# Kernel optimization log

Measured on AMD Instinct MI355X. Metric: run time of the kernel, lower is better.

The kernel has to match this reference:

```python
import jax, jax.numpy as jnp
import numpy as np

BN_EPS = 1e-5


def _weight_mlp(off, Wh, bh, Wo, bo):
    # off: [Nout, k, 2] relative neighbor offsets -> [Nout, k, 9] interp coeffs
    h = jax.nn.relu(off @ Wh + bh)
    return h @ Wo + bo


def _interp_conv(x, idx, off, Wk, bk, Wh, bh, Wo, bo):
    # x: [B, Cin, Nin]; idx: [Nout, k] neighbor indices into Nin; Wk: [Cout, Cin, 9]
    a = _weight_mlp(off, Wh, bh, Wo, bo)        # [Nout, k, 9]
    feats = x[:, :, idx]                         # gather -> [B, Cin, Nout, k]
    # dynamic filter: per-neighbor kernel = a @ Wk taps, contracted with features
    y = jnp.einsum('nkt,bcnk,oct->bon', a, feats, Wk)  # [B, Cout, Nout]
    return y + bk[None, :, None]


def _bn_relu(x, g, b):
    # BatchNorm1d over [B, C, N] using batch statistics (training-mode forward)
    mean = x.mean(axis=(0, 2), keepdims=True)
    var = x.var(axis=(0, 2), keepdims=True)
    xn = (x - mean) * jax.lax.rsqrt(var + BN_EPS)
    return jax.nn.relu(xn * g[None, :, None] + b[None, :, None])


def setup_inputs() -> dict:
    key = jax.random.key(0)
    ks = jax.random.split(key, 12)
    B, N1, N2, N3, K = 8, 50176, 12544, 3136, 9
    inp = {
        'x': jax.random.normal(ks[0], (B, 3, N1), jnp.float32),
        'nbr1': jax.random.randint(ks[1], (N2, K), 0, N1, jnp.int32),
        'off1': jax.random.normal(ks[2], (N2, K, 2), jnp.float32),
        'nbr2': jax.random.randint(ks[3], (N2, K), 0, N2, jnp.int32),
        'off2': jax.random.normal(ks[4], (N2, K, 2), jnp.float32),
        'pool_idx': jax.random.randint(ks[5], (N3, K), 0, N2, jnp.int32),
        'Wh': jax.random.normal(ks[6], (2, 32), jnp.float32) * 0.5,
        'bh': jnp.zeros((32,), jnp.float32),
        'Wo': jax.random.normal(ks[7], (32, 9), jnp.float32) * 0.2,
        'bo': jnp.zeros((9,), jnp.float32),
        'W1': jax.random.normal(ks[8], (32, 3, 9), jnp.float32) * 0.2,
        'b1': jnp.zeros((32,), jnp.float32),
        'W2': jax.random.normal(ks[9], (32, 32, 9), jnp.float32) * 0.06,
        'b2': jnp.zeros((32,), jnp.float32),
        'W3': jax.random.normal(ks[10], (64, 32, 9), jnp.float32) * 0.06,
        'b3': jnp.zeros((64,), jnp.float32),
        'g1': jnp.ones((32,), jnp.float32), 'be1': jnp.zeros((32,), jnp.float32),
        'g2': jnp.ones((32,), jnp.float32), 'be2': jnp.zeros((32,), jnp.float32),
        'g3': jnp.ones((64,), jnp.float32), 'be3': jnp.zeros((64,), jnp.float32),
    }
    return inp


def reference(x, nbr1, off1, nbr2, off2, pool_idx, Wh, bh, Wo, bo,
              W1, b1, W2, b2, W3, b3, g1, be1, g2, be2, g3, be3):
    x = _bn_relu(_interp_conv(x, nbr1, off1, W1, b1, Wh, bh, Wo, bo), g1, be1)
    x = _bn_relu(_interp_conv(x, nbr2, off2, W2, b2, Wh, bh, Wo, bo), g2, be2)
    x = _bn_relu(_interp_conv(x, nbr2, off2, W3, b3, Wh, bh, Wo, bo), g3, be3)
    # MaxPoolNG: max over irregular neighbor sets from level l2 -> l3
    x = x[:, :, pool_idx].max(axis=-1)           # [B, 64, N3]
    return x
```

## Files before the change

kernel.cpp:

```cpp
#include <hip/hip_runtime.h>
#include <math.h>

#define N1C 50176
#define N2C 12544
#define N3C 3136
#define NT_TILES (N2C * 8 / 64)

typedef __attribute__((ext_vector_type(8))) short bf16x8;
typedef __attribute__((ext_vector_type(4))) float f32x4;

__device__ __forceinline__ unsigned short f2bf(float f) {
    unsigned u = __builtin_bit_cast(unsigned, f);
    u += 0x7fffu + ((u >> 16) & 1u);
    return (unsigned short)(u >> 16);
}
__device__ __forceinline__ unsigned cvtpk(float lo, float hi) {
    unsigned r;
    asm("v_cvt_pk_bf16_f32 %0, %1, %2" : "=v"(r) : "v"(lo), "v"(hi));
    return r;
}
__device__ __forceinline__ float bf2f(unsigned short u) {
    return __builtin_bit_cast(float, (unsigned)u << 16);
}
__device__ __forceinline__ float bflo(unsigned u) {
    return __builtin_bit_cast(float, u << 16);
}
__device__ __forceinline__ float bfhi(unsigned u) {
    return __builtin_bit_cast(float, u & 0xffff0000u);
}

#define TRB (N1C / 64)
#define MLB (2 * N2C * 9 / 256)
#define PWB 112

__device__ __forceinline__ void pad_one(int i, const float* __restrict__ W,
                                        unsigned short* __restrict__ Wp,
                                        int OC, int CIN, int KT) {
    int j = i & 7;
    int op = (i >> 3) & 31;
    int q = (i >> 8) & 3;
    int kt = (i >> 10) % KT;
    int g = i / (KT * 1024);
    int kp = kt * 32 + q * 8 + j;
    int t = kp / CIN, c = kp - t * CIN;
    int o = g * 32 + op;
    float v = (t < 9 && o < OC) ? W[(o * CIN + c) * 9 + t] : 0.f;
    Wp[i] = f2bf(v);
}

__global__ void prologue_kernel(const float* __restrict__ x, unsigned short* __restrict__ X0,
                                const float* __restrict__ off1, const float* __restrict__ off2,
                                const float* __restrict__ Wh, const float* __restrict__ bh,
                                const float* __restrict__ Wo, const float* __restrict__ bo,
                                float* __restrict__ A1, float* __restrict__ A2,
                                const float* __restrict__ W1, const float* __restrict__ W2,
                                const float* __restrict__ W3,
                                unsigned short* __restrict__ W1p, unsigned short* __restrict__ W2p,
                                unsigned short* __restrict__ W3p) {
    __shared__ float U[2304];
    int blk = blockIdx.x;
    int tid = threadIdx.x;
    if (blk < TRB) {
        int n0 = blk * 64;
        for (int r = tid; r < 24 * 64; r += 256) {
            int cb = r >> 6;
            int nn = r & 63;
            U[nn * 25 + cb] = x[cb * N1C + n0 + nn];
        }
        __syncthreads();
        for (int w = tid; w < 64 * 24; w += 256) {
            int nn = w / 24;
            int u = w - nn * 24;
            X0[(n0 + nn) * 24 + u] = f2bf(U[nn * 25 + u]);
        }
    } else if (blk < TRB + MLB) {
        int bi = blk - TRB;
        int idx = bi * 256 + tid;
        const float* offp;
        if (idx < N2C * 9) offp = off1 + idx * 2;
        else offp = off2 + (idx - N2C * 9) * 2;
        float o0 = offp[0], o1 = offp[1];
        float out[9];
#pragma unroll
        for (int t = 0; t < 9; t++) out[t] = bo[t];
#pragma unroll
        for (int h = 0; h < 32; h++) {
            float hv = fmaxf(o0 * Wh[h] + o1 * Wh[32 + h] + bh[h], 0.f);
#pragma unroll
            for (int t = 0; t < 9; t++) out[t] += hv * Wo[h * 9 + t];
        }
#pragma unroll
        for (int t = 0; t < 9; t++) U[tid * 9 + t] = out[t];
        __syncthreads();
        float* dst = (bi < 441) ? (A1 + (size_t)bi * 2304)
                                : (A2 + (size_t)(bi - 441) * 2304);
        for (int i = tid; i < 2304; i += 256) dst[i] = U[i];
    } else {
        int i = (blk - TRB - MLB) * 256 + tid;
        if (i < 1024) pad_one(i, W1, W1p, 32, 3, 1);
        else if (i < 10240) pad_one(i - 1024, W2, W2p, 32, 32, 9);
        else pad_one(i - 10240, W3, W3p, 64, 32, 9);
    }
}

template <int CIN, int MW, bool HAS_BN>
__global__ __launch_bounds__(256, 4)
void conv_kernel(const unsigned short* __restrict__ Xin,
                 const int* __restrict__ nbr,
                 const float* __restrict__ A,
                 const unsigned short* __restrict__ Wp,
                 const float* __restrict__ bias,
                 const float* __restrict__ bnsc,
                 const float* __restrict__ bnsh,
                 unsigned short* __restrict__ Yb,
                 double* __restrict__ Part) {
    constexpr int OC = MW * 16;
    constexpr int KREAL = 9 * CIN;
    constexpr int KROW = (KREAL + 31) & ~31;
    constexpr int KT = KROW / 32;
    constexpr int KSTR = KROW + 8;
    constexpr int PARTS = 256 / OC;
    constexpr int PCOLS = 64 / PARTS;
    constexpr int OSH = (OC == 32) ? 5 : 6;
    constexpr int YSTR = OC + 4;
    constexpr int SB1 = 64 * KSTR * 2;
    constexpr int SB2 = 64 * YSTR * 4 + PARTS * 2 * OC * 4;
    constexpr int SBYTES = SB1 > SB2 ? SB1 : SB2;
    __shared__ alignas(16) char Sraw[SBYTES];
    __shared__ float a_lds[8 * 81];
    short* S = (short*)Sraw;

    int tid = threadIdx.x;
    int tile = blockIdx.x;
    int n0 = tile * 8;

    for (int i = tid; i < 64 * KSTR; i += 256) S[i] = 0;
    for (int i = tid; i < 648; i += 256) a_lds[i] = A[(size_t)n0 * 81 + i];
    __syncthreads();
    if (tid < 192) {
        int nsub = tid / 24;
        int u = tid - nsub * 24;
        int b = u / 3, c = u - b * 3;
        int n = n0 + nsub;
        const int* nb = nbr + n * 9;
        const float* Ar = a_lds + nsub * 81;
        float s[9];
#pragma unroll
        for (int t = 0; t < 9; t++) s[t] = 0.f;
#pragma unroll
        for (int k = 0; k < 9; k++) {
            float f = bf2f(Xin[nb[k] * 24 + u]);
#pragma unroll
            for (int t = 0; t < 9; t++) s[t] = fmaf(Ar[k * 9 + t], f, s[t]);
        }
        int col = nsub * 8 + b;
#pragma unroll
        for (int t = 0; t < 9; t++) S[col * KSTR + t * 3 + c] = (short)f2bf(s[t]);
    }
    __syncthreads();

    int lane = tid & 63, wv = tid >> 6, q = lane >> 4, cl = lane & 15;
    int colg = wv * 16 + cl;

    const bf16x8* wf = (const bf16x8*)Wp;
    f32x4 acc[MW];
#pragma unroll
    for (int m = 0; m < MW; m++) acc[m] = (f32x4){0.f, 0.f, 0.f, 0.f};
#pragma unroll
    for (int kt = 0; kt < KT; kt++) {
        bf16x8 bfr = *(const bf16x8*)&S[colg * KSTR + kt * 32 + q * 8];
#pragma unroll
        for (int m = 0; m < MW; m++) {
            const bf16x8* wg = wf + (m >> 1) * (KT * 128);
            bf16x8 am = wg[(kt * 4 + q) * 32 + cl + (m & 1) * 16];
            acc[m] = __builtin_amdgcn_mfma_f32_16x16x32_bf16(am, bfr, acc[m], 0, 0, 0);
        }
    }
    __syncthreads();

    float* Yf = (float*)Sraw;
    float* P2f = Yf + 64 * YSTR;
    int C = tile * 64 + colg;
#pragma unroll
    for (int m = 0; m < MW; m++) {
        f32x4 v;
#pragma unroll
        for (int i = 0; i < 4; i++) v[i] = acc[m][i] + bias[m * 16 + q * 4 + i];
        *(f32x4*)&Yf[colg * YSTR + m * 16 + q * 4] = v;
        uint2 pk;
        pk.x = cvtpk(v[0], v[1]);
        pk.y = cvtpk(v[2], v[3]);
        *(uint2*)&Yb[(size_t)C * OC + m * 16 + q * 4] = pk;
    }
    __syncthreads();
    {
        int o = tid & (OC - 1);
        int part = tid >> OSH;
        float s = 0.f, qq = 0.f;
#pragma unroll
        for (int i = 0; i < PCOLS; i++) {
            float y = Yf[(part * PCOLS + i) * YSTR + o];
            s += y;
            qq += y * y;
        }
        P2f[part * 2 * OC + o] = s;
        P2f[part * 2 * OC + OC + o] = qq;
    }
    __syncthreads();
    if (tid < 2 * OC) {
        double v = 0.0;
#pragma unroll
        for (int p = 0; p < PARTS; p++) v += (double)P2f[p * 2 * OC + tid];
        Part[(size_t)tid * NT_TILES + tile] = v;
    }
}

template <int MW>
__global__ __launch_bounds__(256, 4)
void conv32_kernel(const unsigned short* __restrict__ Xin,
                   const int* __restrict__ nbr,
                   const float* __restrict__ A,
                   const unsigned short* __restrict__ Wp,
                   const float* __restrict__ bias,
                   const float* __restrict__ bnsc,
                   const float* __restrict__ bnsh,
                   unsigned short* __restrict__ Yb,
                   double* __restrict__ Part) {
    constexpr int OC = MW * 16;
    constexpr int KT = 9;
    constexpr int KSTR = 296;
    constexpr int PARTS = 256 / OC;
    constexpr int PCOLS = 64 / PARTS;
    constexpr int OSH = (OC == 32) ? 5 : 6;
    constexpr int YSTR = OC + 4;
    constexpr int SB1 = 64 * KSTR * 2;
    constexpr int SB2 = 64 * YSTR * 4 + PARTS * 2 * OC * 4;
    constexpr int SBYTES = SB1 > SB2 ? SB1 : SB2;
    __shared__ alignas(16) char Sraw[SBYTES];
    __shared__ float a_lds[8 * 81];
    short* S = (short*)Sraw;

    int tid = threadIdx.x;
    int wv4 = __builtin_amdgcn_readfirstlane(tid >> 6);
    int lane = tid & 63;
    int b = lane >> 3, c4 = lane & 7;
    int wv = tid >> 6, q = lane >> 4, cl = lane & 15;
    int colg = wv * 16 + cl;
    float4 scv = *(const float4*)&bnsc[4 * c4];
    float4 shv = *(const float4*)&bnsh[4 * c4];
    const uint2* Xd = (const uint2*)Xin;
    const bf16x8* wf = (const bf16x8*)Wp;
    float* Yf = (float*)Sraw;
    float* P2f = Yf + 64 * YSTR;

#pragma unroll 1
    for (int it = 0; it < 2; ++it) {
        int tile = blockIdx.x * 2 + it;
        int n0 = tile * 8;
        if (it) __syncthreads();

        uint2 fu[18];
#pragma unroll
        for (int gg = 0; gg < 2; gg++)
#pragma unroll
            for (int k = 0; k < 9; k++) {
                int j = nbr[(n0 + wv4 * 2 + gg) * 9 + k];
                fu[gg * 9 + k] = Xd[(size_t)j * 64 + lane];
            }
        for (int i = tid; i < 648; i += 256) a_lds[i] = A[(size_t)n0 * 81 + i];
        __syncthreads();
#pragma unroll
        for (int gg = 0; gg < 2; gg++) {
            const float* Ar = a_lds + (wv4 * 2 + gg) * 81;
            float s0[9], s1[9], s2[9], s3[9];
#pragma unroll
            for (int t = 0; t < 9; t++) { s0[t] = 0.f; s1[t] = 0.f; s2[t] = 0.f; s3[t] = 0.f; }
#pragma unroll
            for (int k = 0; k < 9; k++) {
                uint2 u = fu[gg * 9 + k];
                float f0 = fmaxf(fmaf(bflo(u.x), scv.x, shv.x), 0.f);
                float f1 = fmaxf(fmaf(bfhi(u.x), scv.y, shv.y), 0.f);
                float f2 = fmaxf(fmaf(bflo(u.y), scv.z, shv.z), 0.f);
                float f3 = fmaxf(fmaf(bfhi(u.y), scv.w, shv.w), 0.f);
#pragma unroll
                for (int t = 0; t < 9; t++) {
                    float a = Ar[k * 9 + t];
                    s0[t] = fmaf(a, f0, s0[t]);
                    s1[t] = fmaf(a, f1, s1[t]);
                    s2[t] = fmaf(a, f2, s2[t]);
                    s3[t] = fmaf(a, f3, s3[t]);
                }
            }
            int col = (wv4 * 2 + gg) * 8 + b;
            uint2* Srow = (uint2*)&S[col * KSTR];
#pragma unroll
            for (int t = 0; t < 9; t++) {
                uint2 pk;
                pk.x = cvtpk(s0[t], s1[t]);
                pk.y = cvtpk(s2[t], s3[t]);
                Srow[t * 8 + c4] = pk;
            }
        }
        __syncthreads();

        f32x4 acc[MW];
#pragma unroll
        for (int m = 0; m < MW; m++) acc[m] = (f32x4){0.f, 0.f, 0.f, 0.f};
#pragma unroll
        for (int kt = 0; kt < KT; kt++) {
            bf16x8 bfr = *(const bf16x8*)&S[colg * KSTR + kt * 32 + q * 8];
#pragma unroll
            for (int m = 0; m < MW; m++) {
                const bf16x8* wg = wf + (m >> 1) * (KT * 128);
                bf16x8 am = wg[(kt * 4 + q) * 32 + cl + (m & 1) * 16];
                acc[m] = __builtin_amdgcn_mfma_f32_16x16x32_bf16(am, bfr, acc[m], 0, 0, 0);
            }
        }
        __syncthreads();

        int C = tile * 64 + colg;
#pragma unroll
        for (int m = 0; m < MW; m++) {
            f32x4 v;
#pragma unroll
            for (int i = 0; i < 4; i++) v[i] = acc[m][i] + bias[m * 16 + q * 4 + i];
            *(f32x4*)&Yf[colg * YSTR + m * 16 + q * 4] = v;
            uint2 pk;
            pk.x = cvtpk(v[0], v[1]);
            pk.y = cvtpk(v[2], v[3]);
            *(uint2*)&Yb[(size_t)C * OC + m * 16 + q * 4] = pk;
        }
        __syncthreads();
        {
            int o = tid & (OC - 1);
            int part = tid >> OSH;
            float s = 0.f, qq = 0.f;
#pragma unroll
            for (int i = 0; i < PCOLS; i++) {
                float y = Yf[(part * PCOLS + i) * YSTR + o];
                s += y;
                qq += y * y;
            }
            P2f[part * 2 * OC + o] = s;
            P2f[part * 2 * OC + OC + o] = qq;
        }
        __syncthreads();
        if (tid < 2 * OC) {
            double v = 0.0;
#pragma unroll
            for (int p = 0; p < PARTS; p++) v += (double)P2f[p * 2 * OC + tid];
            Part[(size_t)tid * NT_TILES + tile] = v;
        }
    }
}

__global__ __launch_bounds__(256, 8)
void bn_reduce(const double* __restrict__ Part,
               const float* __restrict__ g, const float* __restrict__ be,
               float* __restrict__ sc, float* __restrict__ sh, int OC) {
    int o = blockIdx.x;
    int tid = threadIdx.x;
    const double* ps = Part + (size_t)o * NT_TILES;
    const double* pq = Part + (size_t)(OC + o) * NT_TILES;
    double s = 0.0, q = 0.0;
    for (int t = tid; t < NT_TILES; t += 256) {
        s += ps[t];
        q += pq[t];
    }
#pragma unroll
    for (int d = 1; d < 64; d <<= 1) {
        s += __shfl_xor(s, d);
        q += __shfl_xor(q, d);
    }
    __shared__ double red[8];
    int wv = tid >> 6;
    if ((tid & 63) == 0) { red[wv] = s; red[4 + wv] = q; }
    __syncthreads();
    if (tid == 0) {
        double S = red[0] + red[1] + red[2] + red[3];
        double Q = red[4] + red[5] + red[6] + red[7];
        double cnt = (double)N2C * 8.0;
        double mean = S / cnt;
        double var = Q / cnt - mean * mean;
        double rs = 1.0 / sqrt(var + 1e-5);
        double scale = (double)g[o] * rs;
        sc[o] = (float)scale;
        sh[o] = (float)((double)be[o] - mean * scale);
    }
}

__global__ __launch_bounds__(256, 8)
void pool_kernel(const unsigned short* __restrict__ Y3, const int* __restrict__ pidx,
                 const float* __restrict__ sc, const float* __restrict__ sh,
                 float* __restrict__ out) {
    int m0 = blockIdx.x * 2;
    int tid = threadIdx.x;
    int o2 = tid & 31;
    int b = tid >> 5;
    float s0 = sc[2 * o2], h0 = sh[2 * o2];
    float s1 = sc[2 * o2 + 1], h1 = sh[2 * o2 + 1];
    const unsigned* Y3u = (const unsigned*)Y3;
    int j0[9], j1[9];
#pragma unroll
    for (int k = 0; k < 9; k++) {
        j0[k] = pidx[m0 * 9 + k];
        j1[k] = pidx[m0 * 9 + 9 + k];
    }
    unsigned u0[9], u1[9];
#pragma unroll
    for (int k = 0; k < 9; k++) u0[k] = Y3u[(size_t)j0[k] * 256 + tid];
#pragma unroll
    for (int k = 0; k < 9; k++) u1[k] = Y3u[(size_t)j1[k] * 256 + tid];
    float a0 = 0.f, a1 = 0.f, c0 = 0.f, c1 = 0.f;
#pragma unroll
    for (int k = 0; k < 9; k++) {
        a0 = fmaxf(a0, fmaf(bflo(u0[k]), s0, h0));
        a1 = fmaxf(a1, fmaf(bfhi(u0[k]), s1, h1));
        c0 = fmaxf(c0, fmaf(bflo(u1[k]), s0, h0));
        c1 = fmaxf(c1, fmaf(bfhi(u1[k]), s1, h1));
    }
    float2 r0 = {a0, c0};
    float2 r1 = {a1, c1};
    *(float2*)(out + (size_t)(b * 64 + 2 * o2) * 3136 + m0) = r0;
    *(float2*)(out + (size_t)(b * 64 + 2 * o2 + 1) * 3136 + m0) = r1;
}

extern "C" void kernel_launch(void* const* d_in, const int* in_sizes, int n_in,
                              void* d_out, int out_size, void* d_ws, size_t ws_size,
                              hipStream_t stream) {
    const float* x    = (const float*)d_in[0];
    const int*   nbr1 = (const int*)d_in[1];
    const float* off1 = (const float*)d_in[2];
    const int*   nbr2 = (const int*)d_in[3];
    const float* off2 = (const float*)d_in[4];
    const int*   pidx = (const int*)d_in[5];
    const float* Wh   = (const float*)d_in[6];
    const float* bh   = (const float*)d_in[7];
    const float* Wo   = (const float*)d_in[8];
    const float* bo   = (const float*)d_in[9];
    const float* W1   = (const float*)d_in[10];
    const float* b1   = (const float*)d_in[11];
    const float* W2   = (const float*)d_in[12];
    const float* b2   = (const float*)d_in[13];
    const float* W3   = (const float*)d_in[14];
    const float* b3   = (const float*)d_in[15];
    const float* g1   = (const float*)d_in[16];
    const float* be1  = (const float*)d_in[17];
    const float* g2   = (const float*)d_in[18];
    const float* be2  = (const float*)d_in[19];
    const float* g3   = (const float*)d_in[20];
    const float* be3  = (const float*)d_in[21];

    char* ws = (char*)d_ws;
    size_t off = 0;
    auto alloc = [&](size_t bytes) -> void* {
        void* p = ws + off;
        off += (bytes + 255) & ~(size_t)255;
        return p;
    };
    unsigned short* X0b = (unsigned short*)alloc((size_t)N1C * 24 * 2);
    float* A1 = (float*)alloc((size_t)N2C * 81 * 4);
    float* A2 = (float*)alloc((size_t)N2C * 81 * 4);
    unsigned short* Y1b = (unsigned short*)alloc((size_t)N2C * 8 * 32 * 2);
    unsigned short* Y2b = (unsigned short*)alloc((size_t)N2C * 8 * 32 * 2);
    unsigned short* Y3b = (unsigned short*)alloc((size_t)N2C * 8 * 64 * 2);
    unsigned short* W1p = (unsigned short*)alloc(32 * 32 * 2);
    unsigned short* W2p = (unsigned short*)alloc(32 * 288 * 2);
    unsigned short* W3p = (unsigned short*)alloc(64 * 288 * 2);
    double* Part  = (double*)alloc((size_t)NT_TILES * 128 * 8);
    float*  scbuf = (float*)alloc(256 * 4);

    float* sc1 = scbuf;       float* sh1 = scbuf + 32;
    float* sc2 = scbuf + 64;  float* sh2 = scbuf + 96;
    float* sc3 = scbuf + 128; float* sh3 = scbuf + 192;

    prologue_kernel<<<TRB + MLB + PWB, 256, 0, stream>>>(
        x, X0b, off1, off2, Wh, bh, Wo, bo, A1, A2, W1, W2, W3, W1p, W2p, W3p);

    conv_kernel<3, 2, false><<<NT_TILES, 256, 0, stream>>>(
        X0b, nbr1, A1, W1p, b1, nullptr, nullptr, Y1b, Part);
    bn_reduce<<<32, 256, 0, stream>>>(Part, g1, be1, sc1, sh1, 32);

    conv32_kernel<2><<<NT_TILES / 2, 256, 0, stream>>>(
        Y1b, nbr2, A2, W2p, b2, sc1, sh1, Y2b, Part);
    bn_reduce<<<32, 256, 0, stream>>>(Part, g2, be2, sc2, sh2, 32);

    conv32_kernel<4><<<NT_TILES / 2, 256, 0, stream>>>(
        Y2b, nbr2, A2, W3p, b3, sc2, sh2, Y3b, Part);
    bn_reduce<<<64, 256, 0, stream>>>(Part, g3, be3, sc3, sh3, 64);

    pool_kernel<<<N3C / 2, 256, 0, stream>>>(Y3b, pidx, sc3, sh3, (float*)d_out);
}
```

Before: 222.9 us.

## Split conv32 into two batch-half launches with 16-point tiles

The 32-channel dynamic-filter convolutions now run as two launches, each handling four of the eight batch images over 16-point tiles, instead of one kernel covering all eight batches over 8-point tiles in a two-iteration loop. Each thread gathers 2 channels for 4 points rather than 4 channels for 2 points. Interpolation coefficients are read straight from global memory instead of being staged in LDS. The aim is a smaller per-launch working set for the gathered features so they stay in cache, plus more reuse of the coefficient matrix per point. In exchange there is an extra launch per layer, narrower 4-byte gather loads, and the coefficient matrix is read twice.

New measurement: 204.3 us. 1.09x faster.

```diff
diff --git a/kernel.cpp b/kernel.cpp
--- a/kernel.cpp
+++ b/kernel.cpp
@@ -5,6 +5,7 @@
 #define N2C 12544
 #define N3C 3136
 #define NT_TILES (N2C * 8 / 64)
+#define BS_TILES (N2C / 16)
 
 typedef __attribute__((ext_vector_type(8))) short bf16x8;
 typedef __attribute__((ext_vector_type(4))) float f32x4;
@@ -215,142 +216,125 @@
     }
 }
 
-template <int MW>
+template <int MW, int B0>
 __global__ __launch_bounds__(256, 4)
-void conv32_kernel(const unsigned short* __restrict__ Xin,
-                   const int* __restrict__ nbr,
-                   const float* __restrict__ A,
-                   const unsigned short* __restrict__ Wp,
-                   const float* __restrict__ bias,
-                   const float* __restrict__ bnsc,
-                   const float* __restrict__ bnsh,
-                   unsigned short* __restrict__ Yb,
-                   double* __restrict__ Part) {
+void conv32_bs(const unsigned short* __restrict__ Xin,
+               const int* __restrict__ nbr,
+               const float* __restrict__ A,
+               const unsigned short* __restrict__ Wp,
+               const float* __restrict__ bias,
+               const float* __restrict__ bnsc,
+               const float* __restrict__ bnsh,
+               unsigned short* __restrict__ Yb,
+               double* __restrict__ Part) {
     constexpr int OC = MW * 16;
-    constexpr int KT = 9;
-    constexpr int KSTR = 296;
     constexpr int PARTS = 256 / OC;
     constexpr int PCOLS = 64 / PARTS;
     constexpr int OSH = (OC == 32) ? 5 : 6;
     constexpr int YSTR = OC + 4;
-    constexpr int SB1 = 64 * KSTR * 2;
-    constexpr int SB2 = 64 * YSTR * 4 + PARTS * 2 * OC * 4;
-    constexpr int SBYTES = SB1 > SB2 ? SB1 : SB2;
-    __shared__ alignas(16) char Sraw[SBYTES];
-    __shared__ float a_lds[8 * 81];
+    constexpr int KSTR = 296;
+    __shared__ alignas(16) char Sraw[64 * KSTR * 2];
     short* S = (short*)Sraw;
 
     int tid = threadIdx.x;
-    int wv4 = __builtin_amdgcn_readfirstlane(tid >> 6);
+    int tile = blockIdx.x;
+    int n0 = tile * 16;
+    int wv = __builtin_amdgcn_readfirstlane(tid >> 6);
     int lane = tid & 63;
-    int b = lane >> 3, c4 = lane & 7;
-    int wv = tid >> 6, q = lane >> 4, cl = lane & 15;
+    int bq = lane >> 4;
+    int c2 = lane & 15;
+    int q = lane >> 4, cl = lane & 15;
     int colg = wv * 16 + cl;
-    float4 scv = *(const float4*)&bnsc[4 * c4];
-    float4 shv = *(const float4*)&bnsh[4 * c4];
-    const uint2* Xd = (const uint2*)Xin;
+
+    float2 scv = *(const float2*)&bnsc[2 * c2];
+    float2 shv = *(const float2*)&bnsh[2 * c2];
+    const unsigned* Xu = (const unsigned*)Xin;
+
+    unsigned fu[36];
+#pragma unroll
+    for (int gg = 0; gg < 4; gg++)
+#pragma unroll
+        for (int k = 0; k < 9; k++) {
+            int j = nbr[(n0 + wv * 4 + gg) * 9 + k];
+            fu[gg * 9 + k] = Xu[((size_t)j * 8 + B0 + bq) * 16 + c2];
+        }
+
+#pragma unroll
+    for (int gg = 0; gg < 4; gg++) {
+        const float* Ar = A + (size_t)(n0 + wv * 4 + gg) * 81;
+        float s0[9], s1[9];
+#pragma unroll
+        for (int t = 0; t < 9; t++) { s0[t] = 0.f; s1[t] = 0.f; }
+#pragma unroll
+        for (int k = 0; k < 9; k++) {
+            unsigned u = fu[gg * 9 + k];
+            float f0 = fmaxf(fmaf(bflo(u), scv.x, shv.x), 0.f);
+            float f1 = fmaxf(fmaf(bfhi(u), scv.y, shv.y), 0.f);
+#pragma unroll
+            for (int t = 0; t < 9; t++) {
+                float a = Ar[k * 9 + t];
+                s0[t] = fmaf(a, f0, s0[t]);
+                s1[t] = fmaf(a, f1, s1[t]);
+            }
+        }
+        int col = (wv * 4 + gg) * 4 + bq;
+        unsigned* Srow = (unsigned*)&S[col * KSTR];
+#pragma unroll
+        for (int t = 0; t < 9; t++) Srow[t * 16 + c2] = cvtpk(s0[t], s1[t]);
+    }
+    __syncthreads();
+
     const bf16x8* wf = (const bf16x8*)Wp;
+    f32x4 acc[MW];
+#pragma unroll
+    for (int m = 0; m < MW; m++) acc[m] = (f32x4){0.f, 0.f, 0.f, 0.f};
+#pragma unroll
+    for (int kt = 0; kt < 9; kt++) {
+        bf16x8 bfr = *(const bf16x8*)&S[colg * KSTR + kt * 32 + q * 8];
+#pragma unroll
+        for (int m = 0; m < MW; m++) {
+            const bf16x8* wg = wf + (m >> 1) * (9 * 128);
+            bf16x8 am = wg[(kt * 4 + q) * 32 + cl + (m & 1) * 16];
+            acc[m] = __builtin_amdgcn_mfma_f32_16x16x32_bf16(am, bfr, acc[m], 0, 0, 0);
+        }
+    }
+    __syncthreads();
+
     float* Yf = (float*)Sraw;
     float* P2f = Yf + 64 * YSTR;
-
-#pragma unroll 1
-    for (int it = 0; it < 2; ++it) {
-        int tile = blockIdx.x * 2 + it;
-        int n0 = tile * 8;
-        if (it) __syncthreads();
-
-        uint2 fu[18];
-#pragma unroll
-        for (int gg = 0; gg < 2; gg++)
-#pragma unroll
-            for (int k = 0; k < 9; k++) {
-                int j = nbr[(n0 + wv4 * 2 + gg) * 9 + k];
-                fu[gg * 9 + k] = Xd[(size_t)j * 64 + lane];
-            }
-        for (int i = tid; i < 648; i += 256) a_lds[i] = A[(size_t)n0 * 81 + i];
-        __syncthreads();
-#pragma unroll
-        for (int gg = 0; gg < 2; gg++) {
-            const float* Ar = a_lds + (wv4 * 2 + gg) * 81;
-            float s0[9], s1[9], s2[9], s3[9];
-#pragma unroll
-            for (int t = 0; t < 9; t++) { s0[t] = 0.f; s1[t] = 0.f; s2[t] = 0.f; s3[t] = 0.f; }
-#pragma unroll
-            for (int k = 0; k < 9; k++) {
-                uint2 u = fu[gg * 9 + k];
-                float f0 = fmaxf(fmaf(bflo(u.x), scv.x, shv.x), 0.f);
-                float f1 = fmaxf(fmaf(bfhi(u.x), scv.y, shv.y), 0.f);
-                float f2 = fmaxf(fmaf(bflo(u.y), scv.z, shv.z), 0.f);
-                float f3 = fmaxf(fmaf(bfhi(u.y), scv.w, shv.w), 0.f);
-#pragma unroll
-                for (int t = 0; t < 9; t++) {
-                    float a = Ar[k * 9 + t];
-                    s0[t] = fmaf(a, f0, s0[t]);
-                    s1[t] = fmaf(a, f1, s1[t]);
-                    s2[t] = fmaf(a, f2, s2[t]);
-                    s3[t] = fmaf(a, f3, s3[t]);
-                }
-            }
-            int col = (wv4 * 2 + gg) * 8 + b;
-            uint2* Srow = (uint2*)&S[col * KSTR];
-#pragma unroll
-            for (int t = 0; t < 9; t++) {
-                uint2 pk;
-                pk.x = cvtpk(s0[t], s1[t]);
-                pk.y = cvtpk(s2[t], s3[t]);
-                Srow[t * 8 + c4] = pk;
-            }
-        }
-        __syncthreads();
-
-        f32x4 acc[MW];
-#pragma unroll
-        for (int m = 0; m < MW; m++) acc[m] = (f32x4){0.f, 0.f, 0.f, 0.f};
-#pragma unroll
-        for (int kt = 0; kt < KT; kt++) {
-            bf16x8 bfr = *(const bf16x8*)&S[colg * KSTR + kt * 32 + q * 8];
-#pragma unroll
-            for (int m = 0; m < MW; m++) {
-                const bf16x8* wg = wf + (m >> 1) * (KT * 128);
-                bf16x8 am = wg[(kt * 4 + q) * 32 + cl + (m & 1) * 16];
-                acc[m] = __builtin_amdgcn_mfma_f32_16x16x32_bf16(am, bfr, acc[m], 0, 0, 0);
-            }
-        }
-        __syncthreads();
-
-        int C = tile * 64 + colg;
-#pragma unroll
-        for (int m = 0; m < MW; m++) {
-            f32x4 v;
-#pragma unroll
-            for (int i = 0; i < 4; i++) v[i] = acc[m][i] + bias[m * 16 + q * 4 + i];
-            *(f32x4*)&Yf[colg * YSTR + m * 16 + q * 4] = v;
-            uint2 pk;
-            pk.x = cvtpk(v[0], v[1]);
-            pk.y = cvtpk(v[2], v[3]);
-            *(uint2*)&Yb[(size_t)C * OC + m * 16 + q * 4] = pk;
-        }
-        __syncthreads();
-        {
-            int o = tid & (OC - 1);
-            int part = tid >> OSH;
-            float s = 0.f, qq = 0.f;
-#pragma unroll
-            for (int i = 0; i < PCOLS; i++) {
-                float y = Yf[(part * PCOLS + i) * YSTR + o];
-                s += y;
-                qq += y * y;
-            }
-            P2f[part * 2 * OC + o] = s;
-            P2f[part * 2 * OC + OC + o] = qq;
-        }
-        __syncthreads();
-        if (tid < 2 * OC) {
-            double v = 0.0;
-#pragma unroll
-            for (int p = 0; p < PARTS; p++) v += (double)P2f[p * 2 * OC + tid];
-            Part[(size_t)tid * NT_TILES + tile] = v;
-        }
+    int nl = colg >> 2, bl = colg & 3;
+    int C = (n0 + nl) * 8 + B0 + bl;
+#pragma unroll
+    for (int m = 0; m < MW; m++) {
+        f32x4 v;
+#pragma unroll
+        for (int i = 0; i < 4; i++) v[i] = acc[m][i] + bias[m * 16 + q * 4 + i];
+        *(f32x4*)&Yf[colg * YSTR + m * 16 + q * 4] = v;
+        uint2 pk;
+        pk.x = cvtpk(v[0], v[1]);
+        pk.y = cvtpk(v[2], v[3]);
+        *(uint2*)&Yb[(size_t)C * OC + m * 16 + q * 4] = pk;
+    }
+    __syncthreads();
+    {
+        int o = tid & (OC - 1);
+        int part = tid >> OSH;
+        float s = 0.f, qq = 0.f;
+#pragma unroll
+        for (int i = 0; i < PCOLS; i++) {
+            float y = Yf[(part * PCOLS + i) * YSTR + o];
+            s += y;
+            qq += y * y;
+        }
+        P2f[part * 2 * OC + o] = s;
+        P2f[part * 2 * OC + OC + o] = qq;
+    }
+    __syncthreads();
+    if (tid < 2 * OC) {
+        double v = 0.0;
+#pragma unroll
+        for (int p = 0; p < PARTS; p++) v += (double)P2f[p * 2 * OC + tid];
+        Part[(size_t)tid * NT_TILES + (B0 / 4) * BS_TILES + tile] = v;
     }
 }
 
@@ -481,11 +465,15 @@
         X0b, nbr1, A1, W1p, b1, nullptr, nullptr, Y1b, Part);
     bn_reduce<<<32, 256, 0, stream>>>(Part, g1, be1, sc1, sh1, 32);
 
-    conv32_kernel<2><<<NT_TILES / 2, 256, 0, stream>>>(
+    conv32_bs<2, 0><<<BS_TILES, 256, 0, stream>>>(
+        Y1b, nbr2, A2, W2p, b2, sc1, sh1, Y2b, Part);
+    conv32_bs<2, 4><<<BS_TILES, 256, 0, stream>>>(
         Y1b, nbr2, A2, W2p, b2, sc1, sh1, Y2b, Part);
     bn_reduce<<<32, 256, 0, stream>>>(Part, g2, be2, sc2, sh2, 32);
 
-    conv32_kernel<4><<<NT_TILES / 2, 256, 0, stream>>>(
+    conv32_bs<4, 0><<<BS_TILES, 256, 0, stream>>>(
+        Y2b, nbr2, A2, W3p, b3, sc2, sh2, Y3b, Part);
+    conv32_bs<4, 4><<<BS_TILES, 256, 0, stream>>>(
         Y2b, nbr2, A2, W3p, b3, sc2, sh2, Y3b, Part);
     bn_reduce<<<64, 256, 0, stream>>>(Part, g3, be3, sc3, sh3, 64);
 
```
